# Performance work log

Measured on AMD Instinct MI355X. Metric: run time of the kernel, lower is better.

## Reference

```python
import jax, jax.numpy as jnp
import numpy as np

N, E, R, D, L, B, K = 50000, 800000, 64, 64, 4, 2, 32


def setup_inputs() -> dict:
    ks = jax.random.split(jax.random.key(0), 10)
    return {
        "edge_index": jax.random.randint(ks[0], (2, E), 0, N),
        "edge_type": jax.random.randint(ks[1], (E,), 0, R),
        "h_index": jax.random.randint(ks[2], (B,), 0, N),
        "r_index": jax.random.randint(ks[3], (B,), 0, R),
        "t_index": jax.random.randint(ks[4], (B, K), 0, N),
        "rel_repr": jax.random.normal(ks[5], (B, R, D)) * 0.1,
        "boundary_extra": jax.random.normal(ks[6], (B, N, D)) * 0.02,
        "layers_W": jax.random.normal(ks[7], (L, 2 * D, D)) / np.sqrt(2 * D),
        "layers_b": jnp.zeros((L, D)),
        "ln_g": jnp.ones((L, D)),
        "ln_b": jnp.zeros((L, D)),
        "w1": jax.random.normal(ks[8], (2 * D, D)) / np.sqrt(2 * D),
        "b1": jnp.zeros((D,)),
        "w2": jax.random.normal(ks[9], (D,)) / np.sqrt(D),
        "b2": jnp.zeros((1,)),
    }


def _layer_norm(x, g, b, eps=1e-5):
    mu = x.mean(-1, keepdims=True)
    var = ((x - mu) ** 2).mean(-1, keepdims=True)
    return (x - mu) * jax.lax.rsqrt(var + eps) * g + b


def reference(edge_index, edge_type, h_index, r_index, t_index, rel_repr,
              boundary_extra, layers_W, layers_b, ln_g, ln_b, w1, b1, w2, b2):
    src, dst = edge_index[0], edge_index[1]
    query = rel_repr[jnp.arange(B), r_index]  # [B, D] per-query relation embedding
    # enhanced boundary: entity/relation-enhanced base + query injected at head node
    boundary = boundary_extra.at[jnp.arange(B), h_index].add(query)  # [B, N, D]
    seg = jax.vmap(lambda m: jax.ops.segment_sum(m, dst, num_segments=N))
    x = boundary
    for l in range(L):
        msg = x[:, src, :] * rel_repr[:, edge_type, :]   # DistMult messages [B, E, D]
        agg = seg(msg) + boundary                        # sum aggregation + boundary self-message
        out = jnp.einsum('bnd,df->bnf', jnp.concatenate([x, agg], -1), layers_W[l]) + layers_b[l]
        out = jax.nn.relu(_layer_norm(out, ln_g[l], ln_b[l]))
        x = out + x                                      # short_cut residual
    node_feat = jnp.concatenate(
        [x, jnp.broadcast_to(query[:, None, :], (B, N, D))], axis=-1)  # [B, N, 2D]
    feat = node_feat[jnp.arange(B)[:, None], t_index]    # gather tails [B, K, 2D]
    h = jax.nn.relu(feat @ w1 + b1)
    score = h @ w2 + b2                                  # [B, K]
    return score
```

## Files before the change

kernel.cpp:

```cpp
#include <hip/hip_runtime.h>
#include <hip/hip_bf16.h>

#define NN 50000
#define EE 800000
#define RR 64
#define DD 64
#define LL 4
#define BB 2
#define KK 32

#define NBUK 98
#define BROWS 512
#define CHUNK 2048
#define NBLK 391
#define PLACE_CAP 10240
#define CAP3 8192

#define PREP_BLKS 196
#define INIT_BLKS 3125
#define HIST_BLKS 391

#define PB_REL   0
#define PB_WT    8192
#define PB_LB    40960
#define PB_G     41216
#define PB_BETA  41472
#define PB_W1    41728
#define PB_B1    49920
#define PB_W2    49984
#define PB_B2    50048
#define PB_TOT   50049

typedef short v8s __attribute__((ext_vector_type(8)));
typedef float v4f __attribute__((ext_vector_type(4)));
typedef _Float16 v2h __attribute__((ext_vector_type(2)));
typedef _Float16 v4h __attribute__((ext_vector_type(4)));
typedef _Float16 v8h __attribute__((ext_vector_type(8)));
typedef unsigned short v4u __attribute__((ext_vector_type(4)));

static __device__ __forceinline__ float ldany(const void* p, int i, int flag) {
    if (flag) return __bfloat162float(((const __hip_bfloat16*)p)[i]);
    return ((const float*)p)[i];
}
static __device__ __forceinline__ unsigned short tobf(float x) {
    return (unsigned short)(__builtin_bit_cast(unsigned int, x) >> 16);
}
static __device__ __forceinline__ unsigned short rnebf(float x) {
    unsigned int u = __builtin_bit_cast(unsigned int, x);
    return (unsigned short)((u + 0x7FFFu + ((u >> 16) & 1u)) >> 16);
}
static __device__ __forceinline__ float frombf(unsigned short h) {
    return __builtin_bit_cast(float, ((unsigned int)h) << 16);
}
static __device__ __forceinline__ int getflag(const unsigned int* lng) {
    return (*lng == 0x3F803F80u) ? 1 : 0;
}

__global__ void __launch_bounds__(256) k_prep(const void* __restrict__ rel, const void* __restrict__ lb,
                       const void* __restrict__ g, const void* __restrict__ beta,
                       const void* __restrict__ w1, const void* __restrict__ b1,
                       const void* __restrict__ w2, const void* __restrict__ b2,
                       const void* __restrict__ W, const unsigned int* __restrict__ lng,
                       const void* __restrict__ be,
                       const int* __restrict__ h_index, const int* __restrict__ r_index,
                       const int* __restrict__ ei,
                       float* __restrict__ pb, unsigned short* __restrict__ wshi,
                       unsigned short* __restrict__ wslo, _Float16* __restrict__ relH,
                       _Float16* __restrict__ xH, int* __restrict__ bucketCount) {
    __shared__ int h[NBUK];
    int blk = blockIdx.x, t = threadIdx.x;
    int flag = getflag(lng);

    if (blk >= PREP_BLKS + INIT_BLKS) {
        if (t < NBUK) h[t] = 0;
        __syncthreads();
        int base = (blk - PREP_BLKS - INIT_BLKS) * CHUNK;
        #pragma unroll
        for (int i = 0; i < 8; ++i) {
            int e = base + i * 256 + t;
            if (e < EE) atomicAdd(&h[ei[EE + e] >> 9], 1);
        }
        __syncthreads();
        if (t < NBUK && h[t]) atomicAdd(&bucketCount[t], h[t]);
        return;
    }
    if (blk >= PREP_BLKS) {
        int gid = (blk - PREP_BLKS) * 256 + t;
        int n = gid >> 4, j = gid & 15, d0 = j * 4;
        float x0[4], x1[4];
        if (flag) {
            v4u a = *(const v4u*)((const unsigned short*)be + (size_t)n * 64 + d0);
            v4u bq = *(const v4u*)((const unsigned short*)be + (size_t)(NN + n) * 64 + d0);
            #pragma unroll
            for (int jj = 0; jj < 4; ++jj) { x0[jj] = frombf(a[jj]); x1[jj] = frombf(bq[jj]); }
        } else {
            v4f a = *(const v4f*)((const float*)be + (size_t)n * 64 + d0);
            v4f bq = *(const v4f*)((const float*)be + (size_t)(NN + n) * 64 + d0);
            #pragma unroll
            for (int jj = 0; jj < 4; ++jj) { x0[jj] = a[jj]; x1[jj] = bq[jj]; }
        }
        if (n == h_index[0]) {
            int r = r_index[0];
            #pragma unroll
            for (int jj = 0; jj < 4; ++jj) x0[jj] += ldany(rel, r * DD + d0 + jj, flag);
        }
        if (n == h_index[1]) {
            int r = r_index[1];
            #pragma unroll
            for (int jj = 0; jj < 4; ++jj) x1[jj] += ldany(rel, (RR + r) * DD + d0 + jj, flag);
        }
        v8h o;
        #pragma unroll
        for (int jj = 0; jj < 4; ++jj) {
            o[2 * jj]     = (_Float16)x0[jj];
            o[2 * jj + 1] = (_Float16)x1[jj];
        }
        *(v8h*)(xH + (size_t)n * 128 + d0 * 2) = o;
        return;
    }

    int gid = blk * 256 + t;
    if (gid < 32768) {
        int l = gid >> 13, r = gid & 8191, f = r >> 7, d = r & 127;
        float w = ldany(W, l * 8192 + d * 64 + f, flag);
        unsigned short h2 = tobf(w);
        wshi[gid] = h2;
        wslo[gid] = tobf(w - frombf(h2));
        if (gid < 8192) {
            int ty = gid >> 7, rr = gid & 127, dd = rr >> 1, b = rr & 1;
            relH[gid] = (_Float16)ldany(rel, b * 4096 + ty * 64 + dd, flag);
        }
    }
    if (gid >= PB_TOT) return;
    if (gid < PB_WT) { pb[gid] = ldany(rel, gid, flag); return; }
    if (gid < PB_LB) return;
    if (gid < PB_G)    { pb[gid] = ldany(lb,   gid - PB_LB,   flag); return; }
    if (gid < PB_BETA) { pb[gid] = ldany(g,    gid - PB_G,    flag); return; }
    if (gid < PB_W1)   { pb[gid] = ldany(beta, gid - PB_BETA, flag); return; }
    if (gid < PB_B1)   { pb[gid] = ldany(w1,   gid - PB_W1,   flag); return; }
    if (gid < PB_W2)   { pb[gid] = ldany(b1,   gid - PB_B1,   flag); return; }
    if (gid < PB_B2)   { pb[gid] = ldany(w2,   gid - PB_W2,   flag); return; }
    pb[gid] = ldany(b2, 0, flag);
}

__global__ void k_bscan(const int* __restrict__ bucketCount,
                        int* __restrict__ bucketBase, int* __restrict__ bucketCursor) {
    __shared__ int s[128];
    int t = threadIdx.x;
    int v = (t < NBUK) ? bucketCount[t] : 0;
    s[t] = v;
    __syncthreads();
    for (int off = 1; off < 128; off <<= 1) {
        int a = (t >= off) ? s[t - off] : 0;
        __syncthreads();
        if (t >= off) s[t] += a;
        __syncthreads();
    }
    if (t < NBUK) {
        int b = s[t] - v;
        bucketBase[t] = b;
        bucketCursor[t] = b;
    }
    if (t == NBUK - 1) bucketBase[NBUK] = s[t];
}

__global__ void __launch_bounds__(256) k_bfill(const int* __restrict__ ei,
                                               const int* __restrict__ et,
                                               int* __restrict__ bucketCursor,
                                               unsigned int* __restrict__ btmp) {
    __shared__ int h[NBUK], rb[NBUK];
    int t = threadIdx.x;
    if (t < NBUK) h[t] = 0;
    __syncthreads();
    int base = blockIdx.x * CHUNK;
    unsigned int rec[8]; int bk[8];
    #pragma unroll
    for (int i = 0; i < 8; ++i) {
        int e = base + i * 256 + t;
        bk[i] = -1;
        if (e < EE) {
            int dst = ei[EE + e];
            rec[i] = (unsigned int)ei[e] | ((unsigned int)et[e] << 16)
                   | ((unsigned int)(dst & 511) << 22);
            bk[i] = dst >> 9;
            atomicAdd(&h[bk[i]], 1);
        }
    }
    __syncthreads();
    if (t < NBUK) rb[t] = h[t] ? atomicAdd(&bucketCursor[t], h[t]) : 0;
    __syncthreads();
    if (t < NBUK) h[t] = 0;
    __syncthreads();
    #pragma unroll
    for (int i = 0; i < 8; ++i) {
        if (bk[i] >= 0) {
            int pos = rb[bk[i]] + atomicAdd(&h[bk[i]], 1);
            btmp[pos] = rec[i];
        }
    }
}

__global__ void __launch_bounds__(256) k_place(const int* __restrict__ bucketBase,
                                               const unsigned int* __restrict__ btmp,
                                               unsigned int* __restrict__ elist,
                                               int* __restrict__ rowptr) {
    __shared__ int rp[BROWS + 1];
    __shared__ int cur[BROWS];
    __shared__ unsigned int outb[PLACE_CAP];
    int b = blockIdx.x, t = threadIdx.x;
    int base = bucketBase[b];
    int cnt  = bucketBase[b + 1] - base;

    for (int r = t; r < BROWS; r += 256) cur[r] = 0;
    __syncthreads();
    for (int i = t; i < cnt; i += 256) {
        unsigned int rec = btmp[base + i];
        atomicAdd(&cur[rec >> 22], 1);
    }
    __syncthreads();
    if (t < 64) {
        int lane = t;
        int loc[8]; int s = 0;
        #pragma unroll
        for (int j = 0; j < 8; ++j) { loc[j] = s; s += cur[lane * 8 + j]; }
        int inc = s;
        for (int off = 1; off < 64; off <<= 1) {
            int v = __shfl_up(inc, off, 64);
            if (lane >= off) inc += v;
        }
        int excl = inc - s;
        #pragma unroll
        for (int j = 0; j < 8; ++j) rp[lane * 8 + j] = excl + loc[j];
        if (lane == 63) rp[BROWS] = inc;
    }
    __syncthreads();
    for (int r = t; r < BROWS; r += 256) cur[r] = rp[r];
    __syncthreads();
    for (int i = t; i < cnt; i += 256) {
        unsigned int rec = btmp[base + i];
        int ld = rec >> 22;
        int pos = atomicAdd(&cur[ld], 1);
        outb[pos] = rec & 0x3FFFFFu;
    }
    __syncthreads();
    for (int i = t; i < cnt; i += 256) elist[base + i] = outb[i];
    for (int r = t; r < BROWS; r += 256) {
        int n = b * BROWS + r;
        if (n <= NN) rowptr[n] = base + rp[r];
    }
}

__global__ void k_sets(const int* __restrict__ t_index,
                       const int* __restrict__ rowptr,
                       const unsigned int* __restrict__ elist,
                       int* __restrict__ flag3,
                       int* __restrict__ listT, int* __restrict__ list3,
                       int* __restrict__ cnts) {
    __shared__ int sT, s3;
    __shared__ int lT[64];
    int t = threadIdx.x;
    if (t == 0) { sT = 0; s3 = 0; }
    __syncthreads();
    if (t < 64) {
        int n = t_index[t];
        if (atomicExch(&flag3[n], 1) == 0) {
            int p = atomicAdd(&sT, 1);
            lT[p] = n; listT[p] = n; list3[p] = n;
        }
    }
    __syncthreads();
    int nT = sT;
    if (t == 0) s3 = nT;
    __syncthreads();
    int wave = t >> 6, lane = t & 63;
    for (int idx = wave; idx < nT; idx += 4) {
        int n = lT[idx];
        int s0 = rowptr[n], s1 = rowptr[n + 1];
        for (int i = s0 + lane; i < s1; i += 64) {
            int src = (int)(elist[i] & 0xFFFFu);
            if (atomicExch(&flag3[src], 1) == 0) {
                int p = atomicAdd(&s3, 1);
                if (p < CAP3) list3[p] = src;
            }
        }
    }
    __syncthreads();
    if (t == 0) { cnts[0] = nT; cnts[1] = (s3 > CAP3) ? CAP3 : s3; }
}

__global__ void __launch_bounds__(256) k_set2(const int* __restrict__ rowptr,
                                              const unsigned int* __restrict__ elist,
                                              const int* __restrict__ list3,
                                              const int* __restrict__ cnt3,
                                              int* __restrict__ flag2,
                                              int* __restrict__ list2,
                                              int* __restrict__ cnt2) {
    int wave = threadIdx.x >> 6, lane = threadIdx.x & 63;
    int nw = gridDim.x * 4;
    int c3 = *cnt3;
    for (int idx = blockIdx.x * 4 + wave; idx < c3; idx += nw) {
        int n = list3[idx];
        if (lane == 0) {
            if (atomicExch(&flag2[n], 1) == 0) list2[atomicAdd(cnt2, 1)] = n;
        }
        int s0 = rowptr[n], s1 = rowptr[n + 1];
        for (int i = s0 + lane; i < s1; i += 64) {
            int src = (int)(elist[i] & 0xFFFFu);
            if (atomicExch(&flag2[src], 1) == 0) {
                list2[atomicAdd(cnt2, 1)] = src;
            }
        }
    }
}

__global__ void __launch_bounds__(256) k_gather(const int* __restrict__ rowptr,
                                                const unsigned int* __restrict__ elist,
                                                const _Float16* __restrict__ xHin,
                                                const _Float16* __restrict__ relH,
                                                const void* __restrict__ be,
                                                const float* __restrict__ relf,
                                                const int* __restrict__ h_index,
                                                const int* __restrict__ r_index,
                                                const unsigned int* __restrict__ lng,
                                                const int* __restrict__ list,
                                                const int* __restrict__ cntp,
                                                unsigned short* __restrict__ aggH) {
    int wave = threadIdx.x >> 6, lane = threadIdx.x & 63;
    int idx = blockIdx.x * 4 + wave;
    int cnt = cntp ? *cntp : NN;
    if (idx >= cnt) return;
    int n = list ? list[idx] : idx;
    n = __builtin_amdgcn_readfirstlane(n);
    int start = __builtin_amdgcn_readfirstlane(rowptr[n]);
    int end   = __builtin_amdgcn_readfirstlane(rowptr[n + 1]);
    int flag  = getflag(lng);

    float a0 = ldany(be, n * DD + lane, flag);
    float a1 = ldany(be, (NN + n) * DD + lane, flag);
    if (n == h_index[0]) a0 += relf[(0 * RR + r_index[0]) * DD + lane];
    if (n == h_index[1]) a1 += relf[(1 * RR + r_index[1]) * DD + lane];

    for (int i = start; i < end; i += 8) {
        v2h xv[8], rv[8]; float mk[8];
        #pragma unroll
        for (int j = 0; j < 8; ++j) {
            int e = i + j;
            int ok = (e < end);
            unsigned int u = elist[ok ? e : start];
            int s = u & 0xFFFFu, ty = u >> 16;
            xv[j] = *(const v2h*)(xHin + s * 128 + lane * 2);
            rv[j] = *(const v2h*)(relH + ty * 128 + lane * 2);
            mk[j] = ok ? 1.f : 0.f;
        }
        #pragma unroll
        for (int j = 0; j < 8; ++j) {
            a0 += (float)xv[j].x * (float)rv[j].x * mk[j];
            a1 += (float)xv[j].y * (float)rv[j].y * mk[j];
        }
    }
    aggH[n * 64 + lane] = rnebf(a0);
    aggH[(NN + n) * 64 + lane] = rnebf(a1);
}

__global__ void __launch_bounds__(256) k_combine(const _Float16* __restrict__ xHin,
                                                 const unsigned short* __restrict__ aggH,
                                                 const unsigned short* __restrict__ whi,
                                                 const unsigned short* __restrict__ wlo,
                                                 const float* __restrict__ lb,
                                                 const float* __restrict__ g,
                                                 const float* __restrict__ beta,
                                                 const int* __restrict__ list,
                                                 const int* __restrict__ cntp,
                                                 _Float16* __restrict__ xHout) {
    __shared__ __attribute__((aligned(16))) unsigned short Xhi[64 * 136];
    __shared__ __attribute__((aligned(16))) unsigned short Xlo[64 * 72];
    __shared__ int nodes[32];
    float* outT = (float*)Xhi;

    int t = threadIdx.x;
    int cnt = cntp ? *cntp : NN;
    int ebase = blockIdx.x * 32;
    if (ebase >= cnt) return;

    if (t < 32) {
        int e = ebase + t;
        int ce = e < cnt ? e : cnt - 1;
        nodes[t] = list ? list[ce] : ce;
    }
    __syncthreads();

    #pragma unroll
    for (int it = 0; it < 4; ++it) {
        int idx = it * 256 + t;
        int nl = idx >> 5, j = idx & 31;
        int n = nodes[nl];
        v4h v = *(const v4h*)(xHin + (size_t)n * 128 + 4 * j);
        int r0 = nl, r1 = 32 + nl;
        int k0 = 2 * j, k1 = 2 * j + 1;
        float f; unsigned short h;
        f = (float)v.x; h = tobf(f); Xhi[r0 * 136 + k0] = h; Xlo[r0 * 72 + k0] = tobf(f - frombf(h));
        f = (float)v.y; h = tobf(f); Xhi[r1 * 136 + k0] = h; Xlo[r1 * 72 + k0] = tobf(f - frombf(h));
        f = (float)v.z; h = tobf(f); Xhi[r0 * 136 + k1] = h; Xlo[r0 * 72 + k1] = tobf(f - frombf(h));
        f = (float)v.w; h = tobf(f); Xhi[r1 * 136 + k1] = h; Xlo[r1 * 72 + k1] = tobf(f - frombf(h));
    }
    #pragma unroll
    for (int it = 0; it < 4; ++it) {
        int idx = it * 256 + t;
        int half = idx >> 9, rem = idx & 511;
        int nl = rem >> 4, j = rem & 15;
        int n = nodes[nl];
        v4u v = *(const v4u*)(aggH + (size_t)(half * NN + n) * 64 + 4 * j);
        int row = half * 32 + nl;
        int kb = 64 + 4 * j;
        Xhi[row * 136 + kb + 0] = v.x;
        Xhi[row * 136 + kb + 1] = v.y;
        Xhi[row * 136 + kb + 2] = v.z;
        Xhi[row * 136 + kb + 3] = v.w;
    }
    __syncthreads();

    int wave = t >> 6, lane = t & 63;
    int low = lane & 15, q = lane >> 4;

    v4f acc[4];
    #pragma unroll
    for (int ft = 0; ft < 4; ++ft) acc[ft] = 0.f;

    int arow = wave * 16 + low;
    #pragma unroll
    for (int kt = 0; kt < 2; ++kt) {
        int k0 = kt * 32 + q * 8;
        v8s ah = *(const v8s*)(Xhi + arow * 136 + k0);
        v8s al = *(const v8s*)(Xlo + arow * 72 + k0);
        #pragma unroll
        for (int ft = 0; ft < 4; ++ft) {
            v8s bh = *(const v8s*)(whi + (ft * 16 + low) * 128 + k0);
            v8s bl = *(const v8s*)(wlo + (ft * 16 + low) * 128 + k0);
            acc[ft] = __builtin_amdgcn_mfma_f32_16x16x32_bf16(ah, bh, acc[ft], 0, 0, 0);
            acc[ft] = __builtin_amdgcn_mfma_f32_16x16x32_bf16(al, bh, acc[ft], 0, 0, 0);
            acc[ft] = __builtin_amdgcn_mfma_f32_16x16x32_bf16(ah, bl, acc[ft], 0, 0, 0);
        }
    }
    #pragma unroll
    for (int kt = 2; kt < 4; ++kt) {
        int k0 = kt * 32 + q * 8;
        v8s ah = *(const v8s*)(Xhi + arow * 136 + k0);
        #pragma unroll
        for (int ft = 0; ft < 4; ++ft) {
            v8s bh = *(const v8s*)(whi + (ft * 16 + low) * 128 + k0);
            v8s bl = *(const v8s*)(wlo + (ft * 16 + low) * 128 + k0);
            acc[ft] = __builtin_amdgcn_mfma_f32_16x16x32_bf16(ah, bh, acc[ft], 0, 0, 0);
            acc[ft] = __builtin_amdgcn_mfma_f32_16x16x32_bf16(ah, bl, acc[ft], 0, 0, 0);
        }
    }

    float o[4][4];
    #pragma unroll
    for (int ft = 0; ft < 4; ++ft) {
        float lbv = lb[ft * 16 + low];
        #pragma unroll
        for (int r = 0; r < 4; ++r) o[ft][r] = acc[ft][r] + lbv;
    }
    float s1[4], s2[4];
    #pragma unroll
    for (int r = 0; r < 4; ++r) {
        s1[r] = o[0][r] + o[1][r] + o[2][r] + o[3][r];
        s2[r] = o[0][r]*o[0][r] + o[1][r]*o[1][r] + o[2][r]*o[2][r] + o[3][r]*o[3][r];
    }
    #pragma unroll
    for (int m = 1; m < 16; m <<= 1) {
        #pragma unroll
        for (int r = 0; r < 4; ++r) {
            s1[r] += __shfl_xor(s1[r], m, 64);
            s2[r] += __shfl_xor(s2[r], m, 64);
        }
    }
    float res[4][4];
    #pragma unroll
    for (int r = 0; r < 4; ++r) {
        int row = wave * 16 + q * 4 + r;
        float mu  = s1[r] * (1.f / 64.f);
        float var = s2[r] * (1.f / 64.f) - mu * mu;
        float rs  = rsqrtf(fmaxf(var, 0.f) + 1e-5f);
        #pragma unroll
        for (int ft = 0; ft < 4; ++ft) {
            int f = ft * 16 + low;
            float xold = frombf(Xhi[row * 136 + f]) + frombf(Xlo[row * 72 + f]);
            res[ft][r] = fmaxf((o[ft][r] - mu) * rs * g[f] + beta[f], 0.f) + xold;
        }
    }
    __syncthreads();

    #pragma unroll
    for (int r = 0; r < 4; ++r) {
        int row = wave * 16 + q * 4 + r;
        #pragma unroll
        for (int ft = 0; ft < 4; ++ft) outT[row * 65 + ft * 16 + low] = res[ft][r];
    }
    __syncthreads();

    #pragma unroll
    for (int it = 0; it < 4; ++it) {
        int idx = it * 256 + t;
        int nl = idx >> 5, j = idx & 31;
        if (ebase + nl < cnt) {
            int n = nodes[nl];
            v4h hv;
            hv.x = (_Float16)outT[nl * 65 + 2 * j];
            hv.y = (_Float16)outT[(32 + nl) * 65 + 2 * j];
            hv.z = (_Float16)outT[nl * 65 + 2 * j + 1];
            hv.w = (_Float16)outT[(32 + nl) * 65 + 2 * j + 1];
            *(v4h*)(xHout + (size_t)n * 128 + 4 * j) = hv;
        }
    }
}

__global__ void k_final(const _Float16* __restrict__ xH,
                        const float* __restrict__ relf,
                        const int* __restrict__ r_index,
                        const int* __restrict__ t_index,
                        const float* __restrict__ w1,
                        const float* __restrict__ b1,
                        const float* __restrict__ w2,
                        const float* __restrict__ b2,
                        const unsigned int* __restrict__ lng,
                        void* __restrict__ out) {
    int b = blockIdx.x >> 5;
    int k = blockIdx.x & 31;
    int f = threadIdx.x;
    int t = t_index[b * KK + k];
    const _Float16* xr = xH + (size_t)t * 128 + b;
    const float* q  = relf + (b * RR + r_index[b]) * DD;
    float acc = b1[f];
    #pragma unroll 8
    for (int d = 0; d < 64; ++d) acc += (float)xr[2 * d] * w1[d * 64 + f];
    #pragma unroll 8
    for (int d = 0; d < 64; ++d) acc += q[d] * w1[(64 + d) * 64 + f];
    float h = fmaxf(acc, 0.f);
    float p = h * w2[f];
    for (int m = 32; m > 0; m >>= 1) p += __shfl_xor(p, m, 64);
    if (f == 0) {
        float s = p + b2[0];
        if (getflag(lng)) ((__hip_bfloat16*)out)[b * KK + k] = __float2bfloat16(s);
        else              ((float*)out)[b * KK + k] = s;
    }
}

extern "C" void kernel_launch(void* const* d_in, const int* in_sizes, int n_in,
                              void* d_out, int out_size, void* d_ws, size_t ws_size,
                              hipStream_t stream) {
    const int* edge_index = (const int*)d_in[0];
    const int* edge_type  = (const int*)d_in[1];
    const int* h_index    = (const int*)d_in[2];
    const int* r_index    = (const int*)d_in[3];
    const int* t_index    = (const int*)d_in[4];
    const void* rel   = d_in[5];
    const void* be    = d_in[6];
    const void* lw    = d_in[7];
    const void* lbias = d_in[8];
    const void* lng   = d_in[9];
    const void* lnb   = d_in[10];
    const void* w1    = d_in[11];
    const void* b1    = d_in[12];
    const void* w2    = d_in[13];
    const void* b2    = d_in[14];

    _Float16* xHa = (_Float16*)d_ws;
    _Float16* xHb = xHa + (size_t)NN * 128;
    unsigned short* aggH = (unsigned short*)(xHb + (size_t)NN * 128);
    float*    pb  = (float*)(aggH + (size_t)BB * NN * 64);
    int*      ip  = (int*)(pb + PB_TOT);
    int* bucketCount = ip;
    int* flag2  = bucketCount + NBUK;
    int* flag3  = flag2 + NN;
    int* cnts   = flag3 + NN;
    int* rowptr = cnts + 16;
    int* bucketBase   = rowptr + NN + 1;
    int* bucketCursor = bucketBase + NBUK + 1;
    int* listT  = bucketCursor + NBUK;
    int* list3  = listT + 64;
    int* list2  = list3 + CAP3;
    unsigned int* elist = (unsigned int*)(list2 + NN);
    unsigned short* wshi = (unsigned short*)(elist + EE);
    unsigned short* wslo = wshi + 32768;
    _Float16* relH = (_Float16*)(wslo + 32768);
    unsigned int* btmp = (unsigned int*)xHb;
    const unsigned int* lngp = (const unsigned int*)lng;

    hipMemsetAsync(bucketCount, 0, (size_t)(NBUK + 2 * NN + 16) * sizeof(int), stream);
    k_prep<<<PREP_BLKS + INIT_BLKS + HIST_BLKS, 256, 0, stream>>>(
        rel, lbias, lng, lnb, w1, b1, w2, b2, lw, lngp, be, h_index, r_index,
        edge_index, pb, wshi, wslo, relH, xHa, bucketCount);
    k_bscan<<<1, 128, 0, stream>>>(bucketCount, bucketBase, bucketCursor);
    k_bfill<<<NBLK, 256, 0, stream>>>(edge_index, edge_type, bucketCursor, btmp);
    k_place<<<NBUK, 256, 0, stream>>>(bucketBase, btmp, elist, rowptr);
    k_sets<<<1, 256, 0, stream>>>(t_index, rowptr, elist, flag3, listT, list3, cnts);
    k_set2<<<256, 256, 0, stream>>>(rowptr, elist, list3, cnts + 1, flag2, list2, cnts + 2);

    const float* relf = pb + PB_REL;
    k_gather<<<12500, 256, 0, stream>>>(rowptr, elist, xHa, relH, be, relf,
                                        h_index, r_index, lngp, nullptr, nullptr, aggH);
    k_combine<<<1563, 256, 0, stream>>>(xHa, aggH, wshi + 0, wslo + 0,
                                        pb + PB_LB + 0, pb + PB_G + 0, pb + PB_BETA + 0,
                                        nullptr, nullptr, xHb);
    k_gather<<<12500, 256, 0, stream>>>(rowptr, elist, xHb, relH, be, relf,
                                        h_index, r_index, lngp, list2, cnts + 2, aggH);
    k_combine<<<1563, 256, 0, stream>>>(xHb, aggH, wshi + 8192, wslo + 8192,
                                        pb + PB_LB + 64, pb + PB_G + 64, pb + PB_BETA + 64,
                                        list2, cnts + 2, xHa);
    k_gather<<<2048, 256, 0, stream>>>(rowptr, elist, xHa, relH, be, relf,
                                       h_index, r_index, lngp, list3, cnts + 1, aggH);
    k_combine<<<256, 256, 0, stream>>>(xHa, aggH, wshi + 16384, wslo + 16384,
                                       pb + PB_LB + 128, pb + PB_G + 128, pb + PB_BETA + 128,
                                       list3, cnts + 1, xHb);
    k_gather<<<16, 256, 0, stream>>>(rowptr, elist, xHb, relH, be, relf,
                                     h_index, r_index, lngp, listT, cnts + 0, aggH);
    k_combine<<<2, 256, 0, stream>>>(xHb, aggH, wshi + 24576, wslo + 24576,
                                     pb + PB_LB + 192, pb + PB_G + 192, pb + PB_BETA + 192,
                                     listT, cnts + 0, xHa);
    k_final<<<64, 64, 0, stream>>>(xHa, pb + PB_REL, r_index, t_index,
                                   pb + PB_W1, pb + PB_B1, pb + PB_W2, pb + PB_B2,
                                   lngp, d_out);
}
```

Measured before the change: 343.3 us.

## Fuse bucket scan into fill/place and fuse last layer with scoring head

Removes the single-block bucket-scan kernel by having every k_bfill and k_place block recompute the 98-entry prefix sum locally from bucketCount. It also replaces the final gather, combine and scoring-head kernels with a single k_tail kernel that aggregates, runs the MFMA layer update, layer norm and residual, then computes scores for the target nodes. A posT mapping built in k_sets links each target to its deduplicated row. This cuts several small launches and their serial gaps, at the cost of redundant scan work in every block and a scoring head handled by only two blocks.

```diff
diff --git a/kernel.cpp b/kernel.cpp
--- a/kernel.cpp
+++ b/kernel.cpp
@@ -143,33 +143,23 @@
     pb[gid] = ldany(b2, 0, flag);
 }
 
-__global__ void k_bscan(const int* __restrict__ bucketCount,
-                        int* __restrict__ bucketBase, int* __restrict__ bucketCursor) {
-    __shared__ int s[128];
-    int t = threadIdx.x;
-    int v = (t < NBUK) ? bucketCount[t] : 0;
-    s[t] = v;
-    __syncthreads();
-    for (int off = 1; off < 128; off <<= 1) {
-        int a = (t >= off) ? s[t - off] : 0;
-        __syncthreads();
-        if (t >= off) s[t] += a;
-        __syncthreads();
-    }
-    if (t < NBUK) {
-        int b = s[t] - v;
-        bucketBase[t] = b;
-        bucketCursor[t] = b;
-    }
-    if (t == NBUK - 1) bucketBase[NBUK] = s[t];
-}
-
 __global__ void __launch_bounds__(256) k_bfill(const int* __restrict__ ei,
                                                const int* __restrict__ et,
-                                               int* __restrict__ bucketCursor,
+                                               const int* __restrict__ bucketCount,
+                                               int* __restrict__ bcur,
                                                unsigned int* __restrict__ btmp) {
-    __shared__ int h[NBUK], rb[NBUK];
+    __shared__ int h[NBUK], rb[NBUK], sb[128];
     int t = threadIdx.x;
+    int v = 0;
+    if (t < 128) { v = (t < NBUK) ? bucketCount[t] : 0; sb[t] = v; }
+    __syncthreads();
+    for (int off = 1; off < 128; off <<= 1) {
+        int a = (t < 128 && t >= off) ? sb[t - off] : 0;
+        __syncthreads();
+        if (t < 128 && t >= off) sb[t] += a;
+        __syncthreads();
+    }
+    if (t < NBUK) sb[t] -= v;
     if (t < NBUK) h[t] = 0;
     __syncthreads();
     int base = blockIdx.x * CHUNK;
@@ -187,7 +177,7 @@
         }
     }
     __syncthreads();
-    if (t < NBUK) rb[t] = h[t] ? atomicAdd(&bucketCursor[t], h[t]) : 0;
+    if (t < NBUK) rb[t] = h[t] ? (sb[t] + atomicAdd(&bcur[t], h[t])) : 0;
     __syncthreads();
     if (t < NBUK) h[t] = 0;
     __syncthreads();
@@ -200,16 +190,29 @@
     }
 }
 
-__global__ void __launch_bounds__(256) k_place(const int* __restrict__ bucketBase,
+__global__ void __launch_bounds__(256) k_place(const int* __restrict__ bucketCount,
                                                const unsigned int* __restrict__ btmp,
                                                unsigned int* __restrict__ elist,
                                                int* __restrict__ rowptr) {
     __shared__ int rp[BROWS + 1];
     __shared__ int cur[BROWS];
     __shared__ unsigned int outb[PLACE_CAP];
+    __shared__ int sb[128];
+    __shared__ int s_base, s_cnt;
     int b = blockIdx.x, t = threadIdx.x;
-    int base = bucketBase[b];
-    int cnt  = bucketBase[b + 1] - base;
+    int v = 0;
+    if (t < 128) { v = (t < NBUK) ? bucketCount[t] : 0; sb[t] = v; }
+    __syncthreads();
+    for (int off = 1; off < 128; off <<= 1) {
+        int a = (t < 128 && t >= off) ? sb[t - off] : 0;
+        __syncthreads();
+        if (t < 128 && t >= off) sb[t] += a;
+        __syncthreads();
+    }
+    if (t == 0) { int cb = bucketCount[b]; s_base = sb[b] - cb; s_cnt = cb; }
+    __syncthreads();
+    int base = s_base;
+    int cnt  = s_cnt;
 
     for (int r = t; r < BROWS; r += 256) cur[r] = 0;
     __syncthreads();
@@ -225,8 +228,8 @@
         for (int j = 0; j < 8; ++j) { loc[j] = s; s += cur[lane * 8 + j]; }
         int inc = s;
         for (int off = 1; off < 64; off <<= 1) {
-            int v = __shfl_up(inc, off, 64);
-            if (lane >= off) inc += v;
+            int vv = __shfl_up(inc, off, 64);
+            if (lane >= off) inc += vv;
         }
         int excl = inc - s;
         #pragma unroll
@@ -254,8 +257,8 @@
                        const int* __restrict__ rowptr,
                        const unsigned int* __restrict__ elist,
                        int* __restrict__ flag3,
-                       int* __restrict__ listT, int* __restrict__ list3,
-                       int* __restrict__ cnts) {
+                       int* __restrict__ listT, int* __restrict__ posT,
+                       int* __restrict__ list3, int* __restrict__ cnts) {
     __shared__ int sT, s3;
     __shared__ int lT[64];
     int t = threadIdx.x;
@@ -272,6 +275,12 @@
     int nT = sT;
     if (t == 0) s3 = nT;
     __syncthreads();
+    if (t < 64) {
+        int n = t_index[t];
+        int p = 0;
+        for (int j = 0; j < nT; ++j) { if (lT[j] == n) { p = j; break; } }
+        posT[t] = p;
+    }
     int wave = t >> 6, lane = t & 63;
     for (int idx = wave; idx < nT; idx += 4) {
         int n = lT[idx];
@@ -515,34 +524,195 @@
     }
 }
 
-__global__ void k_final(const _Float16* __restrict__ xH,
-                        const float* __restrict__ relf,
-                        const int* __restrict__ r_index,
-                        const int* __restrict__ t_index,
-                        const float* __restrict__ w1,
-                        const float* __restrict__ b1,
-                        const float* __restrict__ w2,
-                        const float* __restrict__ b2,
-                        const unsigned int* __restrict__ lng,
-                        void* __restrict__ out) {
-    int b = blockIdx.x >> 5;
-    int k = blockIdx.x & 31;
-    int f = threadIdx.x;
-    int t = t_index[b * KK + k];
-    const _Float16* xr = xH + (size_t)t * 128 + b;
-    const float* q  = relf + (b * RR + r_index[b]) * DD;
-    float acc = b1[f];
-    #pragma unroll 8
-    for (int d = 0; d < 64; ++d) acc += (float)xr[2 * d] * w1[d * 64 + f];
-    #pragma unroll 8
-    for (int d = 0; d < 64; ++d) acc += q[d] * w1[(64 + d) * 64 + f];
-    float h = fmaxf(acc, 0.f);
-    float p = h * w2[f];
-    for (int m = 32; m > 0; m >>= 1) p += __shfl_xor(p, m, 64);
-    if (f == 0) {
-        float s = p + b2[0];
-        if (getflag(lng)) ((__hip_bfloat16*)out)[b * KK + k] = __float2bfloat16(s);
-        else              ((float*)out)[b * KK + k] = s;
+__global__ void __launch_bounds__(256) k_tail(const int* __restrict__ rowptr,
+                                              const unsigned int* __restrict__ elist,
+                                              const _Float16* __restrict__ xHin,
+                                              const _Float16* __restrict__ relH,
+                                              const void* __restrict__ be,
+                                              const float* __restrict__ pb,
+                                              const int* __restrict__ h_index,
+                                              const int* __restrict__ r_index,
+                                              const unsigned int* __restrict__ lng,
+                                              const int* __restrict__ listT,
+                                              const int* __restrict__ posT,
+                                              const int* __restrict__ cnts,
+                                              const unsigned short* __restrict__ whi,
+                                              const unsigned short* __restrict__ wlo,
+                                              const float* __restrict__ lb,
+                                              const float* __restrict__ g,
+                                              const float* __restrict__ beta,
+                                              void* __restrict__ out) {
+    __shared__ __attribute__((aligned(16))) unsigned short Xhi[64 * 136];
+    __shared__ __attribute__((aligned(16))) unsigned short Xlo[64 * 72];
+    __shared__ int nodes[32];
+    float* outT = (float*)Xhi;
+
+    int t = threadIdx.x;
+    int wave = t >> 6, lane = t & 63;
+    int cntT = cnts[0];
+    int ebase = blockIdx.x * 32;
+    if (ebase >= cntT) return;
+    int flag = getflag(lng);
+    const float* relf = pb + PB_REL;
+    int h0 = h_index[0], h1 = h_index[1];
+    int ri0 = r_index[0], ri1 = r_index[1];
+
+    if (t < 32) {
+        int e = ebase + t;
+        int ce = e < cntT ? e : cntT - 1;
+        nodes[t] = listT[ce];
+    }
+    __syncthreads();
+
+    #pragma unroll
+    for (int it = 0; it < 4; ++it) {
+        int idx = it * 256 + t;
+        int nl = idx >> 5, j = idx & 31;
+        int n = nodes[nl];
+        v4h v = *(const v4h*)(xHin + (size_t)n * 128 + 4 * j);
+        int r0 = nl, r1 = 32 + nl;
+        int k0 = 2 * j, k1 = 2 * j + 1;
+        float f; unsigned short h;
+        f = (float)v.x; h = tobf(f); Xhi[r0 * 136 + k0] = h; Xlo[r0 * 72 + k0] = tobf(f - frombf(h));
+        f = (float)v.y; h = tobf(f); Xhi[r1 * 136 + k0] = h; Xlo[r1 * 72 + k0] = tobf(f - frombf(h));
+        f = (float)v.z; h = tobf(f); Xhi[r0 * 136 + k1] = h; Xlo[r0 * 72 + k1] = tobf(f - frombf(h));
+        f = (float)v.w; h = tobf(f); Xhi[r1 * 136 + k1] = h; Xlo[r1 * 72 + k1] = tobf(f - frombf(h));
+    }
+
+    #pragma unroll 1
+    for (int kk = 0; kk < 8; ++kk) {
+        int nl = wave * 8 + kk;
+        if (ebase + nl < cntT) {
+            int n = __builtin_amdgcn_readfirstlane(nodes[nl]);
+            int start = __builtin_amdgcn_readfirstlane(rowptr[n]);
+            int end   = __builtin_amdgcn_readfirstlane(rowptr[n + 1]);
+            float a0 = ldany(be, n * DD + lane, flag);
+            float a1 = ldany(be, (NN + n) * DD + lane, flag);
+            if (n == h0) a0 += relf[ri0 * DD + lane];
+            if (n == h1) a1 += relf[(RR + ri1) * DD + lane];
+            for (int i = start; i < end; i += 8) {
+                v2h xv[8], rv[8]; float mk[8];
+                #pragma unroll
+                for (int j = 0; j < 8; ++j) {
+                    int e = i + j;
+                    int ok = (e < end);
+                    unsigned int u = elist[ok ? e : start];
+                    int s = u & 0xFFFFu, ty = u >> 16;
+                    xv[j] = *(const v2h*)(xHin + s * 128 + lane * 2);
+                    rv[j] = *(const v2h*)(relH + ty * 128 + lane * 2);
+                    mk[j] = ok ? 1.f : 0.f;
+                }
+                #pragma unroll
+                for (int j = 0; j < 8; ++j) {
+                    a0 += (float)xv[j].x * (float)rv[j].x * mk[j];
+                    a1 += (float)xv[j].y * (float)rv[j].y * mk[j];
+                }
+            }
+            Xhi[nl * 136 + 64 + lane] = rnebf(a0);
+            Xhi[(32 + nl) * 136 + 64 + lane] = rnebf(a1);
+        } else {
+            Xhi[nl * 136 + 64 + lane] = 0;
+            Xhi[(32 + nl) * 136 + 64 + lane] = 0;
+        }
+    }
+    __syncthreads();
+
+    int low = lane & 15, q = lane >> 4;
+    v4f acc[4];
+    #pragma unroll
+    for (int ft = 0; ft < 4; ++ft) acc[ft] = 0.f;
+    int arow = wave * 16 + low;
+    #pragma unroll
+    for (int kt = 0; kt < 2; ++kt) {
+        int k0 = kt * 32 + q * 8;
+        v8s ah = *(const v8s*)(Xhi + arow * 136 + k0);
+        v8s al = *(const v8s*)(Xlo + arow * 72 + k0);
+        #pragma unroll
+        for (int ft = 0; ft < 4; ++ft) {
+            v8s bh = *(const v8s*)(whi + (ft * 16 + low) * 128 + k0);
+            v8s bl = *(const v8s*)(wlo + (ft * 16 + low) * 128 + k0);
+            acc[ft] = __builtin_amdgcn_mfma_f32_16x16x32_bf16(ah, bh, acc[ft], 0, 0, 0);
+            acc[ft] = __builtin_amdgcn_mfma_f32_16x16x32_bf16(al, bh, acc[ft], 0, 0, 0);
+            acc[ft] = __builtin_amdgcn_mfma_f32_16x16x32_bf16(ah, bl, acc[ft], 0, 0, 0);
+        }
+    }
+    #pragma unroll
+    for (int kt = 2; kt < 4; ++kt) {
+        int k0 = kt * 32 + q * 8;
+        v8s ah = *(const v8s*)(Xhi + arow * 136 + k0);
+        #pragma unroll
+        for (int ft = 0; ft < 4; ++ft) {
+            v8s bh = *(const v8s*)(whi + (ft * 16 + low) * 128 + k0);
+            v8s bl = *(const v8s*)(wlo + (ft * 16 + low) * 128 + k0);
+            acc[ft] = __builtin_amdgcn_mfma_f32_16x16x32_bf16(ah, bh, acc[ft], 0, 0, 0);
+            acc[ft] = __builtin_amdgcn_mfma_f32_16x16x32_bf16(ah, bl, acc[ft], 0, 0, 0);
+        }
+    }
+    float o[4][4];
+    #pragma unroll
+    for (int ft = 0; ft < 4; ++ft) {
+        float lbv = lb[ft * 16 + low];
+        #pragma unroll
+        for (int r = 0; r < 4; ++r) o[ft][r] = acc[ft][r] + lbv;
+    }
+    float s1[4], s2[4];
+    #pragma unroll
+    for (int r = 0; r < 4; ++r) {
+        s1[r] = o[0][r] + o[1][r] + o[2][r] + o[3][r];
+        s2[r] = o[0][r]*o[0][r] + o[1][r]*o[1][r] + o[2][r]*o[2][r] + o[3][r]*o[3][r];
+    }
+    #pragma unroll
+    for (int m = 1; m < 16; m <<= 1) {
+        #pragma unroll
+        for (int r = 0; r < 4; ++r) {
+            s1[r] += __shfl_xor(s1[r], m, 64);
+            s2[r] += __shfl_xor(s2[r], m, 64);
+        }
+    }
+    float res[4][4];
+    #pragma unroll
+    for (int r = 0; r < 4; ++r) {
+        int row = wave * 16 + q * 4 + r;
+        float mu  = s1[r] * (1.f / 64.f);
+        float var = s2[r] * (1.f / 64.f) - mu * mu;
+        float rs  = rsqrtf(fmaxf(var, 0.f) + 1e-5f);
+        #pragma unroll
+        for (int ft = 0; ft < 4; ++ft) {
+            int f = ft * 16 + low;
+            float xold = frombf(Xhi[row * 136 + f]) + frombf(Xlo[row * 72 + f]);
+            res[ft][r] = fmaxf((o[ft][r] - mu) * rs * g[f] + beta[f], 0.f) + xold;
+        }
+    }
+    __syncthreads();
+    #pragma unroll
+    for (int r = 0; r < 4; ++r) {
+        int row = wave * 16 + q * 4 + r;
+        #pragma unroll
+        for (int ft = 0; ft < 4; ++ft) outT[row * 65 + ft * 16 + low] = res[ft][r];
+    }
+    __syncthreads();
+
+    const float* w1 = pb + PB_W1;
+    for (int j = wave; j < BB * KK; j += 4) {
+        int pj = posT[j];
+        if (pj >= ebase && pj < ebase + 32) {
+            int b = j >> 5, k = j & 31;
+            int row = b * 32 + (pj - ebase);
+            const float* qv = relf + (b * RR + ((b == 0) ? ri0 : ri1)) * DD;
+            float acc2 = pb[PB_B1 + lane];
+            #pragma unroll 8
+            for (int d = 0; d < 64; ++d) acc2 += outT[row * 65 + d] * w1[d * 64 + lane];
+            #pragma unroll 8
+            for (int d = 0; d < 64; ++d) acc2 += qv[d] * w1[(64 + d) * 64 + lane];
+            float hh = fmaxf(acc2, 0.f);
+            float p = hh * pb[PB_W2 + lane];
+            for (int m = 32; m > 0; m >>= 1) p += __shfl_xor(p, m, 64);
+            if (lane == 0) {
+                float s = p + pb[PB_B2];
+                if (flag) ((__hip_bfloat16*)out)[b * KK + k] = __float2bfloat16(s);
+                else      ((float*)out)[b * KK + k] = s;
+            }
+        }
     }
 }
 
@@ -571,14 +741,14 @@
     float*    pb  = (float*)(aggH + (size_t)BB * NN * 64);
     int*      ip  = (int*)(pb + PB_TOT);
     int* bucketCount = ip;
-    int* flag2  = bucketCount + NBUK;
+    int* bcur   = bucketCount + NBUK;
+    int* flag2  = bcur + NBUK;
     int* flag3  = flag2 + NN;
     int* cnts   = flag3 + NN;
     int* rowptr = cnts + 16;
-    int* bucketBase   = rowptr + NN + 1;
-    int* bucketCursor = bucketBase + NBUK + 1;
-    int* listT  = bucketCursor + NBUK;
-    int* list3  = listT + 64;
+    int* listT  = rowptr + NN + 1;
+    int* posT   = listT + 64;
+    int* list3  = posT + 64;
     int* list2  = list3 + CAP3;
     unsigned int* elist = (unsigned int*)(list2 + NN);
     unsigned short* wshi = (unsigned short*)(elist + EE);
@@ -587,14 +757,13 @@
     unsigned int* btmp = (unsigned int*)xHb;
     const unsigned int* lngp = (const unsigned int*)lng;
 
-    hipMemsetAsync(bucketCount, 0, (size_t)(NBUK + 2 * NN + 16) * sizeof(int), stream);
+    hipMemsetAsync(bucketCount, 0, (size_t)(2 * NBUK + 2 * NN + 16) * sizeof(int), stream);
     k_prep<<<PREP_BLKS + INIT_BLKS + HIST_BLKS, 256, 0, stream>>>(
         rel, lbias, lng, lnb, w1, b1, w2, b2, lw, lngp, be, h_index, r_index,
         edge_index, pb, wshi, wslo, relH, xHa, bucketCount);
-    k_bscan<<<1, 128, 0, stream>>>(bucketCount, bucketBase, bucketCursor);
-    k_bfill<<<NBLK, 256, 0, stream>>>(edge_index, edge_type, bucketCursor, btmp);
-    k_place<<<NBUK, 256, 0, stream>>>(bucketBase, btmp, elist, rowptr);
-    k_sets<<<1, 256, 0, stream>>>(t_index, rowptr, elist, flag3, listT, list3, cnts);
+    k_bfill<<<NBLK, 256, 0, stream>>>(edge_index, edge_type, bucketCount, bcur, btmp);
+    k_place<<<NBUK, 256, 0, stream>>>(bucketCount, btmp, elist, rowptr);
+    k_sets<<<1, 256, 0, stream>>>(t_index, rowptr, elist, flag3, listT, posT, list3, cnts);
     k_set2<<<256, 256, 0, stream>>>(rowptr, elist, list3, cnts + 1, flag2, list2, cnts + 2);
 
     const float* relf = pb + PB_REL;
@@ -613,12 +782,9 @@
     k_combine<<<256, 256, 0, stream>>>(xHa, aggH, wshi + 16384, wslo + 16384,
                                        pb + PB_LB + 128, pb + PB_G + 128, pb + PB_BETA + 128,
                                        list3, cnts + 1, xHb);
-    k_gather<<<16, 256, 0, stream>>>(rowptr, elist, xHb, relH, be, relf,
-                                     h_index, r_index, lngp, listT, cnts + 0, aggH);
-    k_combine<<<2, 256, 0, stream>>>(xHb, aggH, wshi + 24576, wslo + 24576,
-                                     pb + PB_LB + 192, pb + PB_G + 192, pb + PB_BETA + 192,
-                                     listT, cnts + 0, xHa);
-    k_final<<<64, 64, 0, stream>>>(xHa, pb + PB_REL, r_index, t_index,
-                                   pb + PB_W1, pb + PB_B1, pb + PB_W2, pb + PB_B2,
-                                   lngp, d_out);
-}
+    k_tail<<<2, 256, 0, stream>>>(rowptr, elist, xHb, relH, be, pb,
+                                  h_index, r_index, lngp, listT, posT, cnts,
+                                  wshi + 24576, wslo + 24576,
+                                  pb + PB_LB + 192, pb + PB_G + 192, pb + PB_BETA + 192,
+                                  d_out);
+}
```

Measured after the change: 377.9 us. 1.1x slower.
